# Performance work log

Hardware: AMD Instinct MI355X
Metric: run time of the kernel (lower is better)

## Reference

```python
import jax, jax.numpy as jnp
import numpy as np

N, E = 50000, 600000
D_IN, D_H, D_OUT, D_E = 128, 128, 128, 32


def setup_inputs() -> dict:
    key = jax.random.key(0)
    ks = jax.random.split(key, 20)
    s = 0.05
    inp = {
        "x": jax.random.normal(ks[0], (N, D_IN), dtype=jnp.float32),
        "edge_index": jax.random.randint(ks[1], (2, E), 0, N, dtype=jnp.int64),
        "edge_attr": jax.random.normal(ks[2], (E, D_E), dtype=jnp.float32),
        # layer 0 (GINEConv MLP + edge lin: edge_dim -> in_channels)
        "w1_0": jax.random.normal(ks[3], (D_IN, D_H), dtype=jnp.float32) * s,
        "b1_0": jnp.zeros((D_H,), jnp.float32),
        "w2_0": jax.random.normal(ks[4], (D_H, D_H), dtype=jnp.float32) * s,
        "b2_0": jnp.zeros((D_H,), jnp.float32),
        "we_0": jax.random.normal(ks[5], (D_E, D_IN), dtype=jnp.float32) * s,
        "be_0": jnp.zeros((D_IN,), jnp.float32),
        # layer 1 (edge lin: edge_dim -> hidden_channels)
        "w1_1": jax.random.normal(ks[6], (D_H, D_H), dtype=jnp.float32) * s,
        "b1_1": jnp.zeros((D_H,), jnp.float32),
        "w2_1": jax.random.normal(ks[7], (D_H, D_H), dtype=jnp.float32) * s,
        "b2_1": jnp.zeros((D_H,), jnp.float32),
        "we_1": jax.random.normal(ks[8], (D_E, D_H), dtype=jnp.float32) * s,
        "be_1": jnp.zeros((D_H,), jnp.float32),
        # output head
        "fc1_w": jax.random.normal(ks[9], (D_H, D_H), dtype=jnp.float32) * s,
        "fc1_b": jnp.zeros((D_H,), jnp.float32),
        "fc2_w": jax.random.normal(ks[10], (D_H, D_OUT), dtype=jnp.float32) * s,
        "fc2_b": jnp.zeros((D_OUT,), jnp.float32),
    }
    return inp


def _gine_layer(x, src, dst, edge_attr, we, be, w1, b1, w2, b2):
    # GINEConv (eps=0): out = MLP(x + sum_j ReLU(x_j + edge_lin(e_ij)))
    e_emb = edge_attr @ we + be                       # [E, d]
    msg = jax.nn.relu(x[src] + e_emb)                 # gather + message
    agg = jax.ops.segment_sum(msg, dst, num_segments=x.shape[0])  # scatter-add
    h = agg + x                                       # (1 + eps) * x, eps = 0
    return jnp.maximum(h @ w1 + b1, 0.0) @ w2 + b2    # 2-layer MLP


def reference(x, edge_index, edge_attr,
              w1_0, b1_0, w2_0, b2_0, we_0, be_0,
              w1_1, b1_1, w2_1, b2_1, we_1, be_1,
              fc1_w, fc1_b, fc2_w, fc2_b):
    src, dst = edge_index[0], edge_index[1]
    h = _gine_layer(x, src, dst, edge_attr, we_0, be_0, w1_0, b1_0, w2_0, b2_0)
    h = jax.nn.relu(h)  # activation (dropout=0 -> identity)
    h = _gine_layer(h, src, dst, edge_attr, we_1, be_1, w1_1, b1_1, w2_1, b2_1)
    h = jax.nn.relu(h)
    h = jax.nn.relu(h @ fc1_w + fc1_b)
    return h @ fc2_w + fc2_b
```

## Files before the change

kernel.cpp:

```cpp
#include <hip/hip_runtime.h>
#include <stdint.h>


#define ND 128
#define ED 32

typedef __attribute__((ext_vector_type(8))) short short8;
typedef __attribute__((ext_vector_type(4))) float f32x4;

__device__ inline unsigned short bf16_hi(float f) {
    union { float f; unsigned u; } v;
    v.f = f;
    return (unsigned short)(v.u >> 16);
}
__device__ inline float bf16_f(unsigned short h) {
    union { unsigned u; float f; } v;
    v.u = ((unsigned)h) << 16;
    return v.f;
}

__global__ __launch_bounds__(256) void zero_kernel(int* __restrict__ p, int n) {
    int i = blockIdx.x * blockDim.x + threadIdx.x;
    if (i < n) p[i] = 0;
}

__global__ __launch_bounds__(256) void hist_kernel(const int* __restrict__ ei,
                                                   int* __restrict__ counts, int E) {
    int i = blockIdx.x * blockDim.x + threadIdx.x;
    if (i < E) atomicAdd(&counts[ei[E + i]], 1);
}

__global__ __launch_bounds__(256) void bsum_kernel(const int* __restrict__ counts,
                                                   int* __restrict__ bsum, int N) {
    __shared__ int s[256];
    int t = threadIdx.x;
    int i = blockIdx.x * 256 + t;
    s[t] = (i < N) ? counts[i] : 0;
    __syncthreads();
#pragma unroll
    for (int off = 128; off > 0; off >>= 1) {
        if (t < off) s[t] += s[t + off];
        __syncthreads();
    }
    if (t == 0) bsum[blockIdx.x] = s[0];
}

__global__ __launch_bounds__(256) void scan_bsums(const int* __restrict__ bsum,
                                                  int* __restrict__ bofs,
                                                  int* __restrict__ row_start_N, int NB) {
    __shared__ int s[256];
    int t = threadIdx.x;
    int chunk = (NB + 255) >> 8;
    int lo = min(t * chunk, NB);
    int hi = min(lo + chunk, NB);
    int sum = 0;
    for (int i = lo; i < hi; ++i) sum += bsum[i];
    s[t] = sum;
    __syncthreads();
    for (int off = 1; off < 256; off <<= 1) {
        int v = (t >= off) ? s[t - off] : 0;
        __syncthreads();
        s[t] += v;
        __syncthreads();
    }
    int pre = (t == 0) ? 0 : s[t - 1];
    for (int i = lo; i < hi; ++i) {
        bofs[i] = pre;
        pre += bsum[i];
    }
    if (t == 255) *row_start_N = s[255];
}

__global__ __launch_bounds__(256) void expand_kernel(const int* __restrict__ counts,
                                                     const int* __restrict__ bofs,
                                                     int* __restrict__ row_start,
                                                     int* __restrict__ woff, int N) {
    __shared__ int s[256];
    int t = threadIdx.x;
    int i = blockIdx.x * 256 + t;
    int c = (i < N) ? counts[i] : 0;
    s[t] = c;
    __syncthreads();
    for (int off = 1; off < 256; off <<= 1) {
        int v = (t >= off) ? s[t - off] : 0;
        __syncthreads();
        s[t] += v;
        __syncthreads();
    }
    if (i < N) {
        int pre = bofs[blockIdx.x] + s[t] - c;
        row_start[i] = pre;
        woff[i] = pre;
    }
}

__global__ __launch_bounds__(256) void scatter_kernel(const int* __restrict__ ei,
                                                      int* __restrict__ woff,
                                                      int2* __restrict__ pack, int E) {
    int i = blockIdx.x * blockDim.x + threadIdx.x;
    if (i < E) {
        int d = ei[E + i];
        int p = atomicAdd(&woff[d], 1);
        pack[p] = make_int2(ei[i], i);
    }
}

__global__ __launch_bounds__(256) void wprep_kernel(
    const float* __restrict__ w0, const float* __restrict__ w1,
    const float* __restrict__ w2, const float* __restrict__ w3,
    const float* __restrict__ w4, const float* __restrict__ w5,
    unsigned short* __restrict__ hi, unsigned short* __restrict__ lo) {
    int t = blockIdx.x * blockDim.x + threadIdx.x;
    const float* W;
    switch (blockIdx.y) {
        case 0: W = w0; break;
        case 1: W = w1; break;
        case 2: W = w2; break;
        case 3: W = w3; break;
        case 4: W = w4; break;
        default: W = w5; break;
    }
    unsigned short* dh = hi + (size_t)blockIdx.y * 16384;
    unsigned short* dl = lo + (size_t)blockIdx.y * 16384;
    int c = t >> 6, l = t & 63;
    int nt = c >> 2, ks = c & 3;
    int n = nt * 16 + (l & 15);
    int kb = ks * 32 + ((l >> 4) << 3);
#pragma unroll
    for (int j = 0; j < 8; ++j) {
        float f = W[(size_t)(kb + j) * ND + n];
        unsigned short h = bf16_hi(f);
        dh[((size_t)c * 64 + l) * 8 + j] = h;
        dl[((size_t)c * 64 + l) * 8 + j] = bf16_hi(f - bf16_f(h));
    }
}

__global__ __launch_bounds__(256) void wprep_we(const float* __restrict__ w0,
                                                const float* __restrict__ w1,
                                                unsigned short* __restrict__ hi) {
    int t = threadIdx.x;
    int c = (blockIdx.x << 2) + (t >> 6);
    int l = t & 63;
    const float* W = blockIdx.y ? w1 : w0;
    unsigned short* dh = hi + (size_t)blockIdx.y * 4096;
    int n = c * 16 + (l & 15);
    int kb = (l >> 4) << 3;
#pragma unroll
    for (int j = 0; j < 8; ++j)
        dh[((size_t)c * 64 + l) * 8 + j] = bf16_hi(W[(size_t)(kb + j) * ND + n]);
}

__global__ __launch_bounds__(256, 4) void agg_mfma(
    const float* __restrict__ xin, const float* __restrict__ edge_attr,
    const unsigned short* __restrict__ bfh, const float* __restrict__ be,
    const int* __restrict__ row_start, const int2* __restrict__ pack,
    float* __restrict__ hout, int N, int NW) {
    int lane = threadIdx.x & 63;
    int gw = (blockIdx.x * blockDim.x + threadIdx.x) >> 6;
    int m = lane & 15;
    int quad = lane >> 4;

    short8 bh[8];
#pragma unroll
    for (int nt = 0; nt < 8; ++nt)
        bh[nt] = *(const short8*)(bfh + ((size_t)nt * 64 + lane) * 8);
    float ber[8];
#pragma unroll
    for (int nt = 0; nt < 8; ++nt) ber[nt] = be[nt * 16 + m];

    for (int v = gw; v < N; v += NW) {
        int beg = row_start[v];
        int end = row_start[v + 1];
        float part[8];
#pragma unroll
        for (int nt = 0; nt < 8; ++nt) part[nt] = 0.f;

        for (int base = beg; base < end; base += 16) {
            int rem = end - base;
            int mm = m < rem ? m : rem - 1;
            int2 pk = pack[base + mm];
            int s[4];
#pragma unroll
            for (int r = 0; r < 4; ++r) s[r] = __shfl(pk.x, quad * 4 + r, 64);

            const float4* ar = (const float4*)(edge_attr + (size_t)pk.y * ED + quad * 8);
            float4 a0 = ar[0], a1 = ar[1];
            float xv[4][8];
#pragma unroll
            for (int r = 0; r < 4; ++r) {
                const float* xr = xin + (size_t)s[r] * ND + m;
#pragma unroll
                for (int nt = 0; nt < 8; ++nt) xv[r][nt] = xr[nt * 16];
            }

            float af[8] = {a0.x, a0.y, a0.z, a0.w, a1.x, a1.y, a1.z, a1.w};
            short8 ah, al;
#pragma unroll
            for (int j = 0; j < 8; ++j) {
                unsigned short h = bf16_hi(af[j]);
                ah[j] = (short)h;
                al[j] = (short)bf16_hi(af[j] - bf16_f(h));
            }

#pragma unroll
            for (int nt = 0; nt < 8; ++nt) {
                f32x4 a = {0.f, 0.f, 0.f, 0.f};
                a = __builtin_amdgcn_mfma_f32_16x16x32_bf16(ah, bh[nt], a, 0, 0, 0);
                a = __builtin_amdgcn_mfma_f32_16x16x32_bf16(al, bh[nt], a, 0, 0, 0);
#pragma unroll
                for (int r = 0; r < 4; ++r) {
                    float vm = (quad * 4 + r) < rem ? 1.f : 0.f;
                    float msg = xv[r][nt] + a[r] + ber[nt];
                    msg = msg > 0.f ? msg : 0.f;
                    part[nt] = fmaf(msg, vm, part[nt]);
                }
            }
        }
#pragma unroll
        for (int nt = 0; nt < 8; ++nt) {
            float p = part[nt];
            p += __shfl_xor(p, 16, 64);
            p += __shfl_xor(p, 32, 64);
            part[nt] = p;
        }
        float o0 = quad == 0 ? part[0] : quad == 1 ? part[2] : quad == 2 ? part[4] : part[6];
        float o1 = quad == 0 ? part[1] : quad == 1 ? part[3] : quad == 2 ? part[5] : part[7];
        int col0 = quad * 32 + m;
        int col1 = col0 + 16;
        hout[(size_t)v * ND + col0] = xin[(size_t)v * ND + col0] + o0;
        hout[(size_t)v * ND + col1] = xin[(size_t)v * ND + col1] + o1;
    }
}

#define LP 132
__global__ __launch_bounds__(512, 4) void mlp2_mfma(
    const float* __restrict__ A,
    const unsigned short* __restrict__ w1h, const unsigned short* __restrict__ w1l,
    const float* __restrict__ b1,
    const unsigned short* __restrict__ w2h, const unsigned short* __restrict__ w2l,
    const float* __restrict__ b2,
    float* __restrict__ C, int N, int relu2) {
    __shared__ float tile[4][16 * LP];
    int t = threadIdx.x;
    int lane = t & 63;
    int wave = t >> 6;
    int pair = wave >> 1;
    int half = wave & 1;
    int m0 = (blockIdx.x * 4 + pair) * 16;
    int m = lane & 15;
    int quad = lane >> 4;
    float* T = tile[pair];

    int row = m0 + m;
    bool rok = row < N;
    short8 ah[4], al[4];
#pragma unroll
    for (int ks = 0; ks < 4; ++ks) {
        float f[8];
        if (rok) {
            const float4* p = (const float4*)(A + (size_t)row * ND + ks * 32 + quad * 8);
            float4 a0 = p[0], a1 = p[1];
            f[0] = a0.x; f[1] = a0.y; f[2] = a0.z; f[3] = a0.w;
            f[4] = a1.x; f[5] = a1.y; f[6] = a1.z; f[7] = a1.w;
        } else {
#pragma unroll
            for (int j = 0; j < 8; ++j) f[j] = 0.f;
        }
#pragma unroll
        for (int j = 0; j < 8; ++j) {
            unsigned short hh = bf16_hi(f[j]);
            ah[ks][j] = (short)hh;
            al[ks][j] = (short)bf16_hi(f[j] - bf16_f(hh));
        }
    }

#pragma unroll
    for (int ntl = 0; ntl < 4; ++ntl) {
        int nt = half * 4 + ntl;
        f32x4 acc = {0.f, 0.f, 0.f, 0.f};
#pragma unroll
        for (int ks = 0; ks < 4; ++ks) {
            size_t off = ((size_t)(nt * 4 + ks) * 64 + lane) * 8;
            short8 bh = *(const short8*)(w1h + off);
            short8 bl = *(const short8*)(w1l + off);
            acc = __builtin_amdgcn_mfma_f32_16x16x32_bf16(ah[ks], bh, acc, 0, 0, 0);
            acc = __builtin_amdgcn_mfma_f32_16x16x32_bf16(al[ks], bh, acc, 0, 0, 0);
            acc = __builtin_amdgcn_mfma_f32_16x16x32_bf16(ah[ks], bl, acc, 0, 0, 0);
        }
        float bv = b1[nt * 16 + m];
#pragma unroll
        for (int r = 0; r < 4; ++r) {
            float o = acc[r] + bv;
            o = o > 0.f ? o : 0.f;
            T[(quad * 4 + r) * LP + nt * 16 + m] = o;
        }
    }

    __syncthreads();

    short8 ch[4], cl[4];
#pragma unroll
    for (int ks = 0; ks < 4; ++ks) {
        const float4* p = (const float4*)(T + m * LP + ks * 32 + quad * 8);
        float4 a0 = p[0], a1 = p[1];
        float f[8] = {a0.x, a0.y, a0.z, a0.w, a1.x, a1.y, a1.z, a1.w};
#pragma unroll
        for (int j = 0; j < 8; ++j) {
            unsigned short hh = bf16_hi(f[j]);
            ch[ks][j] = (short)hh;
            cl[ks][j] = (short)bf16_hi(f[j] - bf16_f(hh));
        }
    }

#pragma unroll
    for (int ntl = 0; ntl < 4; ++ntl) {
        int nt = half * 4 + ntl;
        f32x4 acc = {0.f, 0.f, 0.f, 0.f};
#pragma unroll
        for (int ks = 0; ks < 4; ++ks) {
            size_t off = ((size_t)(nt * 4 + ks) * 64 + lane) * 8;
            short8 bh = *(const short8*)(w2h + off);
            short8 bl = *(const short8*)(w2l + off);
            acc = __builtin_amdgcn_mfma_f32_16x16x32_bf16(ch[ks], bh, acc, 0, 0, 0);
            acc = __builtin_amdgcn_mfma_f32_16x16x32_bf16(cl[ks], bh, acc, 0, 0, 0);
            acc = __builtin_amdgcn_mfma_f32_16x16x32_bf16(ch[ks], bl, acc, 0, 0, 0);
        }
        float bv = b2[nt * 16 + m];
#pragma unroll
        for (int r = 0; r < 4; ++r) {
            int rr = m0 + quad * 4 + r;
            if (rr < N) {
                float o = acc[r] + bv;
                if (relu2) o = o > 0.f ? o : 0.f;
                C[(size_t)rr * ND + nt * 16 + m] = o;
            }
        }
    }
}

extern "C" void kernel_launch(void* const* d_in, const int* in_sizes, int n_in,
                              void* d_out, int out_size, void* d_ws, size_t ws_size,
                              hipStream_t stream) {
    const float* x = (const float*)d_in[0];
    const int* ei = (const int*)d_in[1];
    const float* ea = (const float*)d_in[2];
    const float* w1_0 = (const float*)d_in[3];
    const float* b1_0 = (const float*)d_in[4];
    const float* w2_0 = (const float*)d_in[5];
    const float* b2_0 = (const float*)d_in[6];
    const float* we_0 = (const float*)d_in[7];
    const float* be_0 = (const float*)d_in[8];
    const float* w1_1 = (const float*)d_in[9];
    const float* b1_1 = (const float*)d_in[10];
    const float* w2_1 = (const float*)d_in[11];
    const float* b2_1 = (const float*)d_in[12];
    const float* we_1 = (const float*)d_in[13];
    const float* be_1 = (const float*)d_in[14];
    const float* fc1_w = (const float*)d_in[15];
    const float* fc1_b = (const float*)d_in[16];
    const float* fc2_w = (const float*)d_in[17];
    const float* fc2_b = (const float*)d_in[18];

    int N = in_sizes[0] / ND;
    int E = in_sizes[2] / ED;
    int NB = (N + 255) / 256;

    float* bufA = (float*)d_ws;
    int* counts = (int*)(bufA + (size_t)N * ND);
    int* row_start = counts + N;
    int* woff = row_start + (N + 1);
    int* bsum = woff + N;
    int* bofs = bsum + NB;
    int2* pack = (int2*)((((uintptr_t)(bofs + NB)) + 15) & ~(uintptr_t)15);
    unsigned short* wfh = (unsigned short*)(pack + E);
    unsigned short* wfl = wfh + 6 * 16384;
    unsigned short* weh = wfl + 6 * 16384;
    float* out = (float*)d_out;

    zero_kernel<<<(N + 255) / 256, 256, 0, stream>>>(counts, N);
    hist_kernel<<<(E + 255) / 256, 256, 0, stream>>>(ei, counts, E);
    bsum_kernel<<<NB, 256, 0, stream>>>(counts, bsum, N);
    scan_bsums<<<1, 256, 0, stream>>>(bsum, bofs, row_start + N, NB);
    expand_kernel<<<NB, 256, 0, stream>>>(counts, bofs, row_start, woff, N);
    scatter_kernel<<<(E + 255) / 256, 256, 0, stream>>>(ei, woff, pack, E);
    wprep_kernel<<<dim3(8, 6), 256, 0, stream>>>(w1_0, w2_0, w1_1, w2_1, fc1_w, fc2_w,
                                                 wfh, wfl);
    wprep_we<<<dim3(2, 2), 256, 0, stream>>>(we_0, we_1, weh);

    const int NW = 8192;
    int gg = (N + 63) / 64;

    agg_mfma<<<NW / 4, 256, 0, stream>>>(x, ea, weh, be_0, row_start, pack, out, N, NW);
    mlp2_mfma<<<gg, 512, 0, stream>>>(out, wfh + 0 * 16384, wfl + 0 * 16384, b1_0,
                                      wfh + 1 * 16384, wfl + 1 * 16384, b2_0, bufA, N, 1);

    agg_mfma<<<NW / 4, 256, 0, stream>>>(bufA, ea, weh + 4096, be_1, row_start, pack, out,
                                         N, NW);
    mlp2_mfma<<<gg, 512, 0, stream>>>(out, wfh + 2 * 16384, wfl + 2 * 16384, b1_1,
                                      wfh + 3 * 16384, wfl + 3 * 16384, b2_1, bufA, N, 1);

    mlp2_mfma<<<gg, 512, 0, stream>>>(bufA, wfh + 4 * 16384, wfl + 4 * 16384, fc1_b,
                                      wfh + 5 * 16384, wfl + 5 * 16384, fc2_b, out, N, 0);
}
```

Measured before the change: 483.8 us.

## Split each node's aggregation across two waves by feature half

The edge aggregation kernel now assigns each destination node to a pair of waves, each handling 64 of the 128 feature columns. This halves per-wave registers (weight fragments, gathered x values, partial sums) and doubles the number of waves in flight, improving latency hiding for the irregular gathers. The cost is that each wave pair reloads the edge pack and edge attributes and repeats the bf16 split, so index and edge-feature traffic and some ALU work are duplicated.

```diff
diff --git a/kernel.cpp b/kernel.cpp
--- a/kernel.cpp
+++ b/kernel.cpp
@@ -154,26 +154,28 @@
     const float* __restrict__ xin, const float* __restrict__ edge_attr,
     const unsigned short* __restrict__ bfh, const float* __restrict__ be,
     const int* __restrict__ row_start, const int2* __restrict__ pack,
-    float* __restrict__ hout, int N, int NW) {
+    float* __restrict__ hout, int N, int NWP) {
     int lane = threadIdx.x & 63;
     int gw = (blockIdx.x * blockDim.x + threadIdx.x) >> 6;
+    int wp = gw >> 1;
+    int half = gw & 1;
     int m = lane & 15;
     int quad = lane >> 4;
 
-    short8 bh[8];
-#pragma unroll
-    for (int nt = 0; nt < 8; ++nt)
-        bh[nt] = *(const short8*)(bfh + ((size_t)nt * 64 + lane) * 8);
-    float ber[8];
-#pragma unroll
-    for (int nt = 0; nt < 8; ++nt) ber[nt] = be[nt * 16 + m];
-
-    for (int v = gw; v < N; v += NW) {
+    short8 bh[4];
+#pragma unroll
+    for (int ntl = 0; ntl < 4; ++ntl)
+        bh[ntl] = *(const short8*)(bfh + ((size_t)(half * 4 + ntl) * 64 + lane) * 8);
+    float ber[4];
+#pragma unroll
+    for (int ntl = 0; ntl < 4; ++ntl) ber[ntl] = be[(half * 4 + ntl) * 16 + m];
+
+    for (int v = wp; v < N; v += NWP) {
         int beg = row_start[v];
         int end = row_start[v + 1];
-        float part[8];
-#pragma unroll
-        for (int nt = 0; nt < 8; ++nt) part[nt] = 0.f;
+        float part[4];
+#pragma unroll
+        for (int ntl = 0; ntl < 4; ++ntl) part[ntl] = 0.f;
 
         for (int base = beg; base < end; base += 16) {
             int rem = end - base;
@@ -185,12 +187,12 @@
 
             const float4* ar = (const float4*)(edge_attr + (size_t)pk.y * ED + quad * 8);
             float4 a0 = ar[0], a1 = ar[1];
-            float xv[4][8];
+            float xv[4][4];
 #pragma unroll
             for (int r = 0; r < 4; ++r) {
-                const float* xr = xin + (size_t)s[r] * ND + m;
-#pragma unroll
-                for (int nt = 0; nt < 8; ++nt) xv[r][nt] = xr[nt * 16];
+                const float* xr = xin + (size_t)s[r] * ND + half * 64 + m;
+#pragma unroll
+                for (int ntl = 0; ntl < 4; ++ntl) xv[r][ntl] = xr[ntl * 16];
             }
 
             float af[8] = {a0.x, a0.y, a0.z, a0.w, a1.x, a1.y, a1.z, a1.w};
@@ -203,32 +205,29 @@
             }
 
 #pragma unroll
-            for (int nt = 0; nt < 8; ++nt) {
+            for (int ntl = 0; ntl < 4; ++ntl) {
                 f32x4 a = {0.f, 0.f, 0.f, 0.f};
-                a = __builtin_amdgcn_mfma_f32_16x16x32_bf16(ah, bh[nt], a, 0, 0, 0);
-                a = __builtin_amdgcn_mfma_f32_16x16x32_bf16(al, bh[nt], a, 0, 0, 0);
+                a = __builtin_amdgcn_mfma_f32_16x16x32_bf16(ah, bh[ntl], a, 0, 0, 0);
+                a = __builtin_amdgcn_mfma_f32_16x16x32_bf16(al, bh[ntl], a, 0, 0, 0);
 #pragma unroll
                 for (int r = 0; r < 4; ++r) {
                     float vm = (quad * 4 + r) < rem ? 1.f : 0.f;
-                    float msg = xv[r][nt] + a[r] + ber[nt];
+                    float msg = xv[r][ntl] + a[r] + ber[ntl];
                     msg = msg > 0.f ? msg : 0.f;
-                    part[nt] = fmaf(msg, vm, part[nt]);
+                    part[ntl] = fmaf(msg, vm, part[ntl]);
                 }
             }
         }
 #pragma unroll
-        for (int nt = 0; nt < 8; ++nt) {
-            float p = part[nt];
+        for (int ntl = 0; ntl < 4; ++ntl) {
+            float p = part[ntl];
             p += __shfl_xor(p, 16, 64);
             p += __shfl_xor(p, 32, 64);
-            part[nt] = p;
-        }
-        float o0 = quad == 0 ? part[0] : quad == 1 ? part[2] : quad == 2 ? part[4] : part[6];
-        float o1 = quad == 0 ? part[1] : quad == 1 ? part[3] : quad == 2 ? part[5] : part[7];
-        int col0 = quad * 32 + m;
-        int col1 = col0 + 16;
-        hout[(size_t)v * ND + col0] = xin[(size_t)v * ND + col0] + o0;
-        hout[(size_t)v * ND + col1] = xin[(size_t)v * ND + col1] + o1;
+            part[ntl] = p;
+        }
+        float o = quad == 0 ? part[0] : quad == 1 ? part[1] : quad == 2 ? part[2] : part[3];
+        int col = half * 64 + lane;
+        hout[(size_t)v * ND + col] = xin[(size_t)v * ND + col] + o;
     }
 }
 
@@ -387,15 +386,15 @@
                                                  wfh, wfl);
     wprep_we<<<dim3(2, 2), 256, 0, stream>>>(we_0, we_1, weh);
 
-    const int NW = 8192;
+    const int NWP = 8192;
     int gg = (N + 63) / 64;
 
-    agg_mfma<<<NW / 4, 256, 0, stream>>>(x, ea, weh, be_0, row_start, pack, out, N, NW);
+    agg_mfma<<<NWP / 2, 256, 0, stream>>>(x, ea, weh, be_0, row_start, pack, out, N, NWP);
     mlp2_mfma<<<gg, 512, 0, stream>>>(out, wfh + 0 * 16384, wfl + 0 * 16384, b1_0,
                                       wfh + 1 * 16384, wfl + 1 * 16384, b2_0, bufA, N, 1);
 
-    agg_mfma<<<NW / 4, 256, 0, stream>>>(bufA, ea, weh + 4096, be_1, row_start, pack, out,
-                                         N, NW);
+    agg_mfma<<<NWP / 2, 256, 0, stream>>>(bufA, ea, weh + 4096, be_1, row_start, pack, out,
+                                          N, NWP);
     mlp2_mfma<<<gg, 512, 0, stream>>>(out, wfh + 2 * 16384, wfl + 2 * 16384, b1_1,
                                       wfh + 3 * 16384, wfl + 3 * 16384, b2_1, bufA, N, 1);
 
```

New measurement: 485.6 us. About the same (+0.4%).
